# Performance work log

Measured on AMD Instinct MI355X. Metric: run time of the kernel, lower is better.

Reference implementation:

```python
import jax, jax.numpy as jnp
import numpy as np

N = 32768      # total points (multiple of patch_size -> no padding needed)
C = 768        # channels
H = 8          # num heads
K = 256        # patch_size (window length)
HD = C // H    # head dim = 96, divisible by 6 (3 axes * rotary pairs)
FREQ = 100.0   # rope_freq


def rope3d(x, pos):
    """Point-position RoPE: head dim split into 3 axis chunks, each rotated
    by angles pos_axis * freq**(-i/half).  x: [N,H,HD], pos: [N,3] float."""
    d_axis = HD // 3            # 32
    half = d_axis // 2          # 16
    inv_freq = FREQ ** (-jnp.arange(half, dtype=x.dtype) / half)   # [half]
    ang = pos[:, :, None] * inv_freq[None, None, :]                # [N,3,half]
    cos = jnp.cos(ang)[:, None, :, :]                              # [N,1,3,half]
    sin = jnp.sin(ang)[:, None, :, :]
    xr = x.reshape(x.shape[0], x.shape[1], 3, d_axis)              # [N,H,3,d_axis]
    x1, x2 = xr[..., :half], xr[..., half:]
    out = jnp.concatenate([x1 * cos - x2 * sin, x1 * sin + x2 * cos], axis=-1)
    return out.reshape(x.shape)


def setup_inputs() -> dict:
    key = jax.random.key(0)
    ks = jax.random.split(key, 6)
    feat = jax.random.normal(ks[0], (N, C), dtype=jnp.float32)
    grid_coord = jax.random.randint(ks[1], (N, 3), 0, 1024, dtype=jnp.int32)
    order = jax.random.permutation(ks[2], N).astype(jnp.int32)     # serialized order
    inverse = jnp.argsort(order).astype(jnp.int32)                 # its inverse
    w_qkv = jax.random.normal(ks[3], (C, 3 * C), dtype=jnp.float32) * 0.02
    b_qkv = jnp.zeros((3 * C,), dtype=jnp.float32)
    w_proj = jax.random.normal(ks[4], (C, C), dtype=jnp.float32) * 0.02
    b_proj = jnp.zeros((C,), dtype=jnp.float32)
    return {"feat": feat, "grid_coord": grid_coord, "order": order,
            "inverse": inverse, "w_qkv": w_qkv, "b_qkv": b_qkv,
            "w_proj": w_proj, "b_proj": b_proj}


def reference(feat, grid_coord, order, inverse, w_qkv, b_qkv, w_proj, b_proj):
    scale = HD ** -0.5
    P = N // K  # number of windows
    qkv = (feat @ w_qkv + b_qkv)[order]                   # gather by serialized order
    pos = grid_coord[order].astype(feat.dtype)            # [N,3]
    q, k, v = jnp.split(qkv, 3, axis=-1)
    q = rope3d(q.reshape(N, H, HD), pos)
    k = rope3d(k.reshape(N, H, HD), pos)
    v = v.reshape(N, H, HD)
    # windowed (varlen with equal patch lengths) attention
    qw = q.reshape(P, K, H, HD)
    kw = k.reshape(P, K, H, HD)
    vw = v.reshape(P, K, H, HD)
    logits = jnp.einsum('pqhd,pkhd->phqk', qw, kw) * scale
    attn = jax.nn.softmax(logits, axis=-1)
    out = jnp.einsum('phqk,pkhd->pqhd', attn, vw).reshape(N, C)
    out = out[inverse]                                    # scatter back to input order
    return out @ w_proj + b_proj
```

## Files before the change

### kernel.cpp

```cpp
#include <hip/hip_runtime.h>
#include <hip/hip_bf16.h>
#include <stdint.h>

typedef __bf16 bf16_t;
typedef __bf16 bf16x8 __attribute__((ext_vector_type(8)));
typedef __bf16 bf16x4 __attribute__((ext_vector_type(4)));
typedef float f32x4 __attribute__((ext_vector_type(4)));

template <int V> struct ic { static constexpr int value = V; };

__device__ __forceinline__ void gload_lds16(const bf16_t* g, bf16_t* l) {
  __builtin_amdgcn_global_load_lds((const __attribute__((address_space(1))) void*)g,
                                   (__attribute__((address_space(3))) void*)l, 16, 0, 0);
}

__global__ __launch_bounds__(256) void transpose_cast_k(const float* __restrict__ W,
                                                        bf16_t* __restrict__ Bt,
                                                        int KDin, int MDin) {
  __shared__ float tile[64][65];
  const int bm = blockIdx.x, bk = blockIdx.y;
  const int c = threadIdx.x & 63, r0 = threadIdx.x >> 6;
#pragma unroll
  for (int rr = 0; rr < 16; ++rr) {
    int row = rr * 4 + r0;
    tile[row][c] = W[(size_t)(bk * 64 + row) * MDin + bm * 64 + c];
  }
  __syncthreads();
#pragma unroll
  for (int rr = 0; rr < 16; ++rr) {
    int mo = rr * 4 + r0;
    Bt[(size_t)(bm * 64 + mo) * KDin + bk * 64 + c] = (bf16_t)tile[c][mo];
  }
}

__global__ __launch_bounds__(256) void gather_cast_k(const float* __restrict__ feat,
                                                     const int* __restrict__ order,
                                                     const int* __restrict__ grid_coord,
                                                     bf16_t* __restrict__ featp,
                                                     float* __restrict__ posf) {
  const int id = blockIdx.x * 256 + threadIdx.x;
  const int j = id / 192;
  const int c = (id % 192) * 4;
  const int g = order[j];
  const float4 v = *(const float4*)(feat + (size_t)g * 768 + c);
  bf16x4 o;
  o[0] = (bf16_t)v.x; o[1] = (bf16_t)v.y; o[2] = (bf16_t)v.z; o[3] = (bf16_t)v.w;
  *(bf16x4*)(featp + (size_t)j * 768 + c) = o;
  if (c == 0) {
    posf[j * 3 + 0] = (float)grid_coord[g * 3 + 0];
    posf[j * 3 + 1] = (float)grid_coord[g * 3 + 1];
    posf[j * 3 + 2] = (float)grid_coord[g * 3 + 2];
  }
}

template <int MODE, int NBX>
__global__ __launch_bounds__(512, 2) void gemm256_k(const bf16_t* __restrict__ A,
                                                    const bf16_t* __restrict__ Bt,
                                                    const float* __restrict__ bias,
                                                    bf16_t* __restrict__ Cq,
                                                    bf16_t* __restrict__ Ck,
                                                    bf16_t* __restrict__ Cv,
                                                    float* __restrict__ Cf,
                                                    const int* __restrict__ order,
                                                    const float* __restrict__ posf) {
  extern __shared__ bf16_t sm[];
  bf16_t* ldsA = sm;
  bf16_t* ldsB = sm + 4 * 8192;

  const int tid = threadIdx.x;
  const int lane = tid & 63, wave = tid >> 6;
  const int wr = wave >> 2, wc = wave & 3;
  const int lq = lane & 15, lk = lane >> 4;

  const int bid = blockIdx.x;
  const int cpx = gridDim.x >> 3;
  const int rm = (bid & 7) * cpx + (bid >> 3);
  const int by = rm / NBX, bx = rm % NBX;

  const int o0 = tid, o1 = tid + 512;
  const int r0s = o0 >> 2, ls0 = (o0 & 3) ^ ((r0s >> 1) & 3);
  const int r1s = o1 >> 2, ls1 = (o1 & 3) ^ ((r1s >> 1) & 3);
  const bf16_t* pA0 = A + (size_t)(by * 256 + r0s) * 768 + ls0 * 8;
  const bf16_t* pA1 = A + (size_t)(by * 256 + r1s) * 768 + ls1 * 8;
  const bf16_t* pB0 = Bt + (size_t)(bx * 256 + r0s) * 768 + ls0 * 8;
  const bf16_t* pB1 = Bt + (size_t)(bx * 256 + r1s) * 768 + ls1 * 8;

  auto stageA = [&](int kt) {
    bf16_t* d = ldsA + ((kt & 3) << 13);
    gload_lds16(pA0 + kt * 32, d + o0 * 8);
    gload_lds16(pA1 + kt * 32, d + o1 * 8);
  };
  auto stageB = [&](int kt) {
    bf16_t* d = ldsB + ((kt & 3) << 13);
    gload_lds16(pB0 + kt * 32, d + o0 * 8);
    gload_lds16(pB1 + kt * 32, d + o1 * 8);
  };

  const int pslot = lk ^ ((lq >> 1) & 3);

  f32x4 acc[8][4] = {};

  stageA(0); stageB(0); stageA(1); stageB(1); stageA(2); stageB(2);
  asm volatile("s_waitcnt vmcnt(8)" ::: "memory");
  __builtin_amdgcn_s_barrier();
  __builtin_amdgcn_sched_barrier(0);

  auto group = [&](int t, auto VMC, auto STGC) {
    constexpr int VM = decltype(VMC)::value;
    constexpr bool STG = decltype(STGC)::value;
    const bf16_t* Ab = ldsA + ((t & 3) << 13);
    const bf16_t* Bb = ldsB + ((t & 3) << 13);
    bf16x8 af[4], bfr[4];
#pragma unroll
    for (int m = 0; m < 4; ++m)
      af[m] = *(const bf16x8*)(Ab + (wr * 128 + m * 16 + lq) * 32 + pslot * 8);
#pragma unroll
    for (int n = 0; n < 4; ++n)
      bfr[n] = *(const bf16x8*)(Bb + (wc * 64 + n * 16 + lq) * 32 + pslot * 8);
    if constexpr (STG) stageA(t + 3);
    __builtin_amdgcn_s_barrier();
    asm volatile("s_waitcnt lgkmcnt(0)" ::: "memory");
    __builtin_amdgcn_s_setprio(1);
#pragma unroll
    for (int n = 0; n < 4; ++n)
#pragma unroll
      for (int m = 0; m < 4; ++m)
        acc[m][n] = __builtin_amdgcn_mfma_f32_16x16x32_bf16(af[m], bfr[n], acc[m][n], 0, 0, 0);
    __builtin_amdgcn_s_setprio(0);
    __builtin_amdgcn_s_barrier();
#pragma unroll
    for (int m = 0; m < 4; ++m)
      af[m] = *(const bf16x8*)(Ab + (wr * 128 + 64 + m * 16 + lq) * 32 + pslot * 8);
    if constexpr (STG) stageB(t + 3);
    if constexpr (VM == 8) asm volatile("s_waitcnt vmcnt(8)" ::: "memory");
    else if constexpr (VM == 4) asm volatile("s_waitcnt vmcnt(4)" ::: "memory");
    else if constexpr (VM == 0) asm volatile("s_waitcnt vmcnt(0)" ::: "memory");
    __builtin_amdgcn_s_barrier();
    asm volatile("s_waitcnt lgkmcnt(0)" ::: "memory");
    __builtin_amdgcn_s_setprio(1);
#pragma unroll
    for (int n = 0; n < 4; ++n)
#pragma unroll
      for (int m = 0; m < 4; ++m)
        acc[4 + m][n] = __builtin_amdgcn_mfma_f32_16x16x32_bf16(af[m], bfr[n], acc[4 + m][n], 0, 0, 0);
    __builtin_amdgcn_s_setprio(0);
    __builtin_amdgcn_s_barrier();
    __builtin_amdgcn_sched_barrier(0);
  };

  for (int t = 0; t < 21; ++t) group(t, ic<8>{}, ic<1>{});
  group(21, ic<4>{}, ic<0>{});
  group(22, ic<0>{}, ic<0>{});
  group(23, ic<-1>{}, ic<0>{});

  const int colb = bx * 256 + wc * 64;
  float bcol[4];
#pragma unroll
  for (int n = 0; n < 4; ++n) bcol[n] = bias[colb + n * 16 + lq];

  if (MODE == 0) {
    const int sec = bx / 3;
    const int coll = colb - sec * 768;
    if (sec < 2) {
      bf16_t* base = sec == 0 ? Cq : Ck;
      const int a0 = (colb % 96) >> 5;
      const int a1 = ((colb + 32) % 96) >> 5;
      const float fr = exp2f(-0.41524101186f * (float)lq);
#pragma unroll
      for (int m = 0; m < 8; ++m) {
        const int rowb = by * 256 + wr * 128 + m * 16 + lk * 4;
#pragma unroll
        for (int r = 0; r < 4; ++r) {
          const int row = rowb + r;
          float s0, c0, s1, c1;
          __sincosf(posf[row * 3 + a0] * fr, &s0, &c0);
          __sincosf(posf[row * 3 + a1] * fr, &s1, &c1);
          const float x1 = acc[m][0][r] + bcol[0], x2 = acc[m][1][r] + bcol[1];
          const float y1 = acc[m][2][r] + bcol[2], y2 = acc[m][3][r] + bcol[3];
          acc[m][0][r] = x1 * c0 - x2 * s0;
          acc[m][1][r] = x1 * s0 + x2 * c0;
          acc[m][2][r] = y1 * c1 - y2 * s1;
          acc[m][3][r] = y1 * s1 + y2 * c1;
        }
#pragma unroll
        for (int n = 0; n < 4; ++n) {
          const int col = coll + n * 16 + lq;
#pragma unroll
          for (int r = 0; r < 4; ++r)
            base[(size_t)(rowb + r) * 768 + col] = (bf16_t)acc[m][n][r];
        }
      }
    } else {
#pragma unroll
      for (int m = 0; m < 8; ++m) {
        const int rowb = by * 256 + wr * 128 + m * 16 + lk * 4;
#pragma unroll
        for (int n = 0; n < 4; ++n) {
          const int col = coll + n * 16 + lq;
          bf16x4 o;
#pragma unroll
          for (int r = 0; r < 4; ++r) o[r] = (bf16_t)(acc[m][n][r] + bcol[n]);
          *(bf16x4*)(Cv + (size_t)col * 32768 + rowb) = o;
        }
      }
    }
  } else {
#pragma unroll
    for (int m = 0; m < 8; ++m) {
      const int rowb = by * 256 + wr * 128 + m * 16 + lk * 4;
      int ro[4];
#pragma unroll
      for (int r = 0; r < 4; ++r) ro[r] = order[rowb + r];
#pragma unroll
      for (int n = 0; n < 4; ++n) {
        const int col = colb + n * 16 + lq;
#pragma unroll
        for (int r = 0; r < 4; ++r)
          Cf[(size_t)ro[r] * 768 + col] = acc[m][n][r] + bcol[n];
      }
    }
  }
}

__global__ __launch_bounds__(512) void attn_k(bf16_t* QO,
                                              const bf16_t* __restrict__ Kb,
                                              const bf16_t* __restrict__ Vt) {
  extern __shared__ bf16_t alds[];
  bf16_t* Kreg = alds;
  bf16_t* Vreg = alds + 24576;
  const int bid = blockIdx.x;
  const int h = bid & 7, p = bid >> 3;
  const int tid = threadIdx.x, lane = tid & 63, wave = tid >> 6;
  const int lq = lane & 15, lk = lane >> 4;
  const int tok0 = p * 256;
  const float scale = 0.10206207262f;
  bf16_t* pw = alds + 49152 + wave * 2048;

  bf16x8 aq[2][3];
#pragma unroll
  for (int rb = 0; rb < 2; ++rb) {
    const bf16_t* qb = QO + (size_t)(tok0 + wave * 32 + rb * 16 + lq) * 768 + h * 96 + lk * 8;
#pragma unroll
    for (int kc = 0; kc < 3; ++kc) aq[rb][kc] = *(const bf16x8*)(qb + kc * 32);
  }
  __builtin_amdgcn_sched_barrier(0);

#pragma unroll
  for (int i = 0; i < 6; ++i) {
    const int fi = i * 8 + wave;
    const int nt = fi / 3, a = fi - nt * 3;
    const bf16_t* src = Kb + (size_t)(tok0 + nt * 16 + (lane & 15)) * 768 +
                        h * 96 + a * 32 + (lane >> 4) * 8;
    gload_lds16(src, Kreg + i * 4096 + tid * 8);
  }
#pragma unroll
  for (int i = 0; i < 6; ++i) {
    const int fi = i * 8 + wave;
    const int d = (fi >> 3) * 16 + (lane & 15);
    const int tb = (fi & 7) * 32 + (lane >> 4) * 8;
    const bf16_t* src = Vt + (size_t)(h * 96 + d) * 32768 + tok0 + tb;
    gload_lds16(src, Vreg + i * 4096 + tid * 8);
  }

  asm volatile("s_waitcnt vmcnt(6)" ::: "memory");
  __builtin_amdgcn_s_barrier();

#pragma unroll
  for (int rb = 0; rb < 2; ++rb) {
    f32x4 sacc[16];
#pragma unroll
    for (int nt = 0; nt < 16; ++nt) {
      f32x4 acc = {0.f, 0.f, 0.f, 0.f};
#pragma unroll
      for (int kc = 0; kc < 3; ++kc) {
        bf16x8 bk = *(const bf16x8*)(Kreg + (size_t)((nt * 3 + kc) * 64 + lane) * 8);
        acc = __builtin_amdgcn_mfma_f32_16x16x32_bf16(aq[rb][kc], bk, acc, 0, 0, 0);
      }
      sacc[nt] = acc;
    }

    float linv[4];
#pragma unroll
    for (int r = 0; r < 4; ++r) {
      float mx = -1e30f;
#pragma unroll
      for (int nt = 0; nt < 16; ++nt) mx = fmaxf(mx, sacc[nt][r]);
      mx = fmaxf(mx, __shfl_xor(mx, 1));
      mx = fmaxf(mx, __shfl_xor(mx, 2));
      mx = fmaxf(mx, __shfl_xor(mx, 4));
      mx = fmaxf(mx, __shfl_xor(mx, 8));
      mx *= scale;
      float l = 0.f;
#pragma unroll
      for (int nt = 0; nt < 16; ++nt) {
        float e = __expf(sacc[nt][r] * scale - mx);
        sacc[nt][r] = e;
        l += e;
      }
      l += __shfl_xor(l, 1);
      l += __shfl_xor(l, 2);
      l += __shfl_xor(l, 4);
      l += __shfl_xor(l, 8);
      linv[r] = 1.f / l;
    }

    if (rb == 0) {
      asm volatile("s_waitcnt vmcnt(0)" ::: "memory");
      __builtin_amdgcn_s_barrier();
    }

    f32x4 oacc[6] = {};
#pragma unroll
    for (int hf = 0; hf < 2; ++hf) {
#pragma unroll
      for (int ntl = 0; ntl < 8; ++ntl) {
        const int nt = hf * 8 + ntl;
        const int chk = ntl * 2 + (lq >> 3);
#pragma unroll
        for (int r = 0; r < 4; ++r) {
          const int row = lk * 4 + r;
          const int phys = chk ^ (row & 7);
          pw[row * 128 + phys * 8 + (lq & 7)] = (bf16_t)sacc[nt][r];
        }
      }
#pragma unroll
      for (int kcl = 0; kcl < 4; ++kcl) {
        const int physr = (kcl * 4 + lk) ^ (lq & 7);
        bf16x8 pf = *(const bf16x8*)(pw + lq * 128 + physr * 8);
        const int kc = hf * 4 + kcl;
#pragma unroll
        for (int dt = 0; dt < 6; ++dt) {
          bf16x8 vb = *(const bf16x8*)(Vreg + (size_t)((dt * 8 + kc) * 64 + lane) * 8);
          oacc[dt] = __builtin_amdgcn_mfma_f32_16x16x32_bf16(pf, vb, oacc[dt], 0, 0, 0);
        }
      }
    }

#pragma unroll
    for (int dt = 0; dt < 6; ++dt) {
#pragma unroll
      for (int r = 0; r < 4; ++r) {
        const int row = tok0 + wave * 32 + rb * 16 + lk * 4 + r;
        QO[(size_t)row * 768 + h * 96 + dt * 16 + lq] = (bf16_t)(oacc[dt][r] * linv[r]);
      }
    }
  }
}

extern "C" void kernel_launch(void* const* d_in, const int* in_sizes, int n_in,
                              void* d_out, int out_size, void* d_ws, size_t ws_size,
                              hipStream_t stream) {
  const float* feat       = (const float*)d_in[0];
  const int*   grid_coord = (const int*)d_in[1];
  const int*   order      = (const int*)d_in[2];
  const float* w_qkv      = (const float*)d_in[4];
  const float* b_qkv      = (const float*)d_in[5];
  const float* w_proj     = (const float*)d_in[6];
  const float* b_proj     = (const float*)d_in[7];
  float* out = (float*)d_out;

  char* ws = (char*)d_ws;
  bf16_t* Bt1   = (bf16_t*)(ws);
  bf16_t* Bt2   = (bf16_t*)(ws + 3538944);
  bf16_t* featp = (bf16_t*)(ws + 4718592);
  bf16_t* Qb    = (bf16_t*)(ws + 55050240);
  bf16_t* Kb    = (bf16_t*)(ws + 105381888);
  bf16_t* Vt    = (bf16_t*)(ws + 155713536);
  float*  posf  = (float*)(ws + 206045184);

  static bool attr_set = false;
  if (!attr_set) {
    (void)hipFuncSetAttribute((const void*)gemm256_k<0, 9>,
                              hipFuncAttributeMaxDynamicSharedMemorySize, 131072);
    (void)hipFuncSetAttribute((const void*)gemm256_k<1, 3>,
                              hipFuncAttributeMaxDynamicSharedMemorySize, 131072);
    (void)hipFuncSetAttribute((const void*)attn_k,
                              hipFuncAttributeMaxDynamicSharedMemorySize, 131072);
    attr_set = true;
  }

  transpose_cast_k<<<dim3(36, 12), 256, 0, stream>>>(w_qkv, Bt1, 768, 2304);
  transpose_cast_k<<<dim3(12, 12), 256, 0, stream>>>(w_proj, Bt2, 768, 768);
  gather_cast_k<<<24576, 256, 0, stream>>>(feat, order, grid_coord, featp, posf);
  gemm256_k<0, 9><<<1152, 512, 131072, stream>>>(featp, Bt1, b_qkv, Qb, Kb, Vt,
                                                 nullptr, nullptr, posf);
  attn_k<<<1024, 512, 131072, stream>>>(Qb, Kb, Vt);
  gemm256_k<1, 3><<<384, 512, 131072, stream>>>(Qb, Bt2, b_proj, nullptr, nullptr,
                                                nullptr, out, order, nullptr);
}
```

Measured before the change: 484.3 us.

## Add dedicated 128x256-tile projection GEMM with gathered A rows via inverse

Replaces the 256x256-tile output projection GEMM with a new kernel using 128x256 tiles, a 4-slot LDS pipeline and 96KB of shared memory, launching 768 blocks with two blocks per CU allowed. Instead of scattering output rows through order, it gathers input A rows through inverse, so the output stores become contiguous. The aim is better occupancy and load balance for the small projection GEMM and cheaper coalesced writes, at the cost of reading A rows indirectly.

```diff
diff --git a/kernel.cpp b/kernel.cpp
--- a/kernel.cpp
+++ b/kernel.cpp
@@ -222,6 +222,102 @@
   }
 }
 
+__global__ __launch_bounds__(512, 2) void gemm_proj_k(const bf16_t* __restrict__ A,
+                                                      const bf16_t* __restrict__ Bt,
+                                                      const float* __restrict__ bias,
+                                                      float* __restrict__ Cf,
+                                                      const int* __restrict__ inverse) {
+  extern __shared__ bf16_t sm[];
+  bf16_t* ldsA = sm;
+  bf16_t* ldsB = sm + 16384;
+
+  const int tid = threadIdx.x;
+  const int lane = tid & 63, wave = tid >> 6;
+  const int wr = wave >> 2, wc = wave & 3;
+  const int lq = lane & 15, lk = lane >> 4;
+
+  const int bid = blockIdx.x;
+  const int cpx = gridDim.x >> 3;
+  const int rm = (bid & 7) * cpx + (bid >> 3);
+  const int by = rm / 3, bx = rm % 3;
+
+  const int rA = tid >> 2, lsA = (tid & 3) ^ ((rA >> 1) & 3);
+  const int gA = inverse[by * 128 + rA];
+  const bf16_t* pA = A + (size_t)gA * 768 + lsA * 8;
+  const int o0 = tid, o1 = tid + 512;
+  const int rB0 = o0 >> 2, lsB0 = (o0 & 3) ^ ((rB0 >> 1) & 3);
+  const int rB1 = o1 >> 2, lsB1 = (o1 & 3) ^ ((rB1 >> 1) & 3);
+  const bf16_t* pB0 = Bt + (size_t)(bx * 256 + rB0) * 768 + lsB0 * 8;
+  const bf16_t* pB1 = Bt + (size_t)(bx * 256 + rB1) * 768 + lsB1 * 8;
+
+  auto stage = [&](int kt) {
+    const int slot = kt & 3;
+    gload_lds16(pA + kt * 32, ldsA + (slot << 12) + tid * 8);
+    gload_lds16(pB0 + kt * 32, ldsB + (slot << 13) + o0 * 8);
+    gload_lds16(pB1 + kt * 32, ldsB + (slot << 13) + o1 * 8);
+  };
+
+  const int pslot = lk ^ ((lq >> 1) & 3);
+
+  f32x4 acc[4][4] = {};
+
+  stage(0); stage(1); stage(2);
+  asm volatile("s_waitcnt vmcnt(6)" ::: "memory");
+  __builtin_amdgcn_s_barrier();
+  __builtin_amdgcn_sched_barrier(0);
+
+  auto group = [&](int t, auto VMC, auto STGC) {
+    constexpr int VM = decltype(VMC)::value;
+    constexpr bool STG = decltype(STGC)::value;
+    const bf16_t* Ab = ldsA + ((t & 3) << 12);
+    const bf16_t* Bb = ldsB + ((t & 3) << 13);
+    bf16x8 af[4], bfr[4];
+#pragma unroll
+    for (int m = 0; m < 4; ++m)
+      af[m] = *(const bf16x8*)(Ab + (wr * 64 + m * 16 + lq) * 32 + pslot * 8);
+#pragma unroll
+    for (int n = 0; n < 4; ++n)
+      bfr[n] = *(const bf16x8*)(Bb + (wc * 64 + n * 16 + lq) * 32 + pslot * 8);
+    if constexpr (STG) stage(t + 3);
+    if constexpr (VM == 6) asm volatile("s_waitcnt vmcnt(6)" ::: "memory");
+    else if constexpr (VM == 3) asm volatile("s_waitcnt vmcnt(3)" ::: "memory");
+    else if constexpr (VM == 0) asm volatile("s_waitcnt vmcnt(0)" ::: "memory");
+    __builtin_amdgcn_s_barrier();
+    asm volatile("s_waitcnt lgkmcnt(0)" ::: "memory");
+    __builtin_amdgcn_sched_barrier(0);
+    __builtin_amdgcn_s_setprio(1);
+#pragma unroll
+    for (int n = 0; n < 4; ++n)
+#pragma unroll
+      for (int m = 0; m < 4; ++m)
+        acc[m][n] = __builtin_amdgcn_mfma_f32_16x16x32_bf16(af[m], bfr[n], acc[m][n], 0, 0, 0);
+    __builtin_amdgcn_s_setprio(0);
+    __builtin_amdgcn_s_barrier();
+    __builtin_amdgcn_sched_barrier(0);
+  };
+
+  for (int t = 0; t < 21; ++t) group(t, ic<6>{}, ic<1>{});
+  group(21, ic<3>{}, ic<0>{});
+  group(22, ic<0>{}, ic<0>{});
+  group(23, ic<-1>{}, ic<0>{});
+
+  const int colb = bx * 256 + wc * 64;
+  float bcol[4];
+#pragma unroll
+  for (int n = 0; n < 4; ++n) bcol[n] = bias[colb + n * 16 + lq];
+#pragma unroll
+  for (int m = 0; m < 4; ++m) {
+    const int rowb = by * 128 + wr * 64 + m * 16 + lk * 4;
+#pragma unroll
+    for (int n = 0; n < 4; ++n) {
+      const int col = colb + n * 16 + lq;
+#pragma unroll
+      for (int r = 0; r < 4; ++r)
+        Cf[(size_t)(rowb + r) * 768 + col] = acc[m][n][r] + bcol[n];
+    }
+  }
+}
+
 __global__ __launch_bounds__(512) void attn_k(bf16_t* QO,
                                               const bf16_t* __restrict__ Kb,
                                               const bf16_t* __restrict__ Vt) {
@@ -353,6 +449,7 @@
   const float* feat       = (const float*)d_in[0];
   const int*   grid_coord = (const int*)d_in[1];
   const int*   order      = (const int*)d_in[2];
+  const int*   inverse    = (const int*)d_in[3];
   const float* w_qkv      = (const float*)d_in[4];
   const float* b_qkv      = (const float*)d_in[5];
   const float* w_proj     = (const float*)d_in[6];
@@ -372,8 +469,8 @@
   if (!attr_set) {
     (void)hipFuncSetAttribute((const void*)gemm256_k<0, 9>,
                               hipFuncAttributeMaxDynamicSharedMemorySize, 131072);
-    (void)hipFuncSetAttribute((const void*)gemm256_k<1, 3>,
-                              hipFuncAttributeMaxDynamicSharedMemorySize, 131072);
+    (void)hipFuncSetAttribute((const void*)gemm_proj_k,
+                              hipFuncAttributeMaxDynamicSharedMemorySize, 98304);
     (void)hipFuncSetAttribute((const void*)attn_k,
                               hipFuncAttributeMaxDynamicSharedMemorySize, 131072);
     attr_set = true;
@@ -385,6 +482,5 @@
   gemm256_k<0, 9><<<1152, 512, 131072, stream>>>(featp, Bt1, b_qkv, Qb, Kb, Vt,
                                                  nullptr, nullptr, posf);
   attn_k<<<1024, 512, 131072, stream>>>(Qb, Kb, Vt);
-  gemm256_k<1, 3><<<384, 512, 131072, stream>>>(Qb, Bt2, b_proj, nullptr, nullptr,
-                                                nullptr, out, order, nullptr);
-}
+  gemm_proj_k<<<768, 512, 98304, stream>>>(Qb, Bt2, b_proj, out, inverse);
+}
```

Measured after the change: 478.6 us. No clear change (-1.2%).
